# Kernel optimization log

Measured on AMD Instinct MI355X. Metric: run time of the kernel, lower is better.

The kernel has to match this reference:

```python
import jax, jax.numpy as jnp
import numpy as np

K = 5          # k = min(5, min(S, T)) with S = T = 4096
SIGMA = 1.0
EPS_VAR = 1e-08
EPS_LOG = 1e-08


def _entropy(p):
    # sum(-p * log2(clamp(p, 1e-8)), axis=1).mean()
    return jnp.sum(-p * jnp.log2(jnp.clip(p, EPS_LOG, None)), axis=1).mean()


def _pairwise_dist(x):
    # Euclidean cdist via GEMM (matches torch's use_mm_for_euclid path)
    sq = jnp.sum(x * x, axis=1)                       # [N]
    d2 = sq[:, None] + sq[None, :] - 2.0 * (x @ x.T)  # [N, N]
    d2 = jnp.maximum(d2, 0.0)
    # safe sqrt (zero diagonal) — value identical, grad-safe
    return jnp.where(d2 > 0, jnp.sqrt(jnp.where(d2 > 0, d2, 1.0)), 0.0)


def _row_var(block):
    # sqrt(k-th smallest distance per row + eps): max of k smallest
    kth = -jax.lax.top_k(-block, K)[0][:, -1]
    return jnp.sqrt(kth + EPS_VAR)                    # [rows]


def _sim(block, var_row, zero_diag):
    s = jnp.exp(-block / (2.0 * (var_row[:, None] * SIGMA) ** 2))
    if zero_diag:
        n = block.shape[0]
        s = s * (1.0 - jnp.eye(n, dtype=s.dtype))
    return s


def _forward(Feature_all, logit_all, y_source):
    S = y_source.shape[0]
    logit_source = logit_all[:S]
    logit_target = logit_all[S:]

    # cross-entropy on source
    logp = jax.nn.log_softmax(logit_source, axis=1)
    loss_cl = -jnp.take_along_axis(logp, y_source[:, None], axis=1).mean()

    # entropy of target softmax
    loss_ce = _entropy(jax.nn.softmax(logit_target, axis=1))

    # reg_loss_dist
    dist = _pairwise_dist(Feature_all)                # [N, N]
    d_ss = dist[:S, :S]
    d_st = dist[:S, S:]
    d_tt = dist[S:, S:]
    d_ts = dist[S:, :S]

    sim_ss = _sim(d_ss, _row_var(d_ss), True)
    sim_st = _sim(d_st, _row_var(d_st), False)
    sim_tt = _sim(d_tt, _row_var(d_tt), True)
    sim_ts = _sim(d_ts, _row_var(d_ts), False)

    src_intra = jnp.max(sim_ss, axis=1)
    src_inter = jnp.max(sim_st, axis=1)
    tgt_intra = jnp.max(sim_tt, axis=1)
    tgt_inter = jnp.max(sim_ts, axis=1)

    loss_reg = (jnp.abs(src_intra - src_inter).mean()
                + jnp.abs(tgt_intra - tgt_inter).mean())
    return loss_cl, loss_ce, loss_reg


def setup_inputs() -> dict:
    key = jax.random.key(0)
    k1, k2, k3 = jax.random.split(key, 3)
    N, D, C, S = 8192, 256, 65, 4096
    return {
        "Feature_all": jax.random.normal(k1, (N, D), dtype=jnp.float32),
        "logit_all": jax.random.normal(k2, (N, C), dtype=jnp.float32),
        "y_source": jax.random.randint(k3, (S,), 0, C, dtype=jnp.int64
                                       if jax.config.jax_enable_x64 else jnp.int32),
        "device": 0,
    }


def reference(Feature_all, logit_all, y_source, device):
    del device  # torch-specific, ignored
    return _forward(Feature_all, logit_all, y_source)
```

## Files before the change

### kernel.cpp

```cpp
#include <hip/hip_runtime.h>
#include <stdint.h>

#define Nn 8192
#define Dd 256
#define Ss 4096
#define Cc 65

#define TI 128
#define TJ 128
#define BK 32
#define CHUNK 1024
#define NCHUNK (Nn / CHUNK)
#define NJT (CHUNK / TJ)
#define KS (Dd / BK)

#define BIGF 3.0e37f

typedef float f4 __attribute__((ext_vector_type(4)));
typedef __bf16 bf8 __attribute__((ext_vector_type(8)));

__device__ __forceinline__ float wredsum(float v) {
#pragma unroll
  for (int o = 32; o; o >>= 1) v += __shfl_xor(v, o, 64);
  return v;
}
__device__ __forceinline__ float wredmax(float v) {
#pragma unroll
  for (int o = 32; o; o >>= 1) v = fmaxf(v, __shfl_xor(v, o, 64));
  return v;
}

__device__ __forceinline__ unsigned short f2bf(float f) {
  unsigned int u = __float_as_uint(f);
  u = (u + 0x7fffu + ((u >> 16) & 1u)) >> 16;
  return (unsigned short)u;
}

__device__ __forceinline__ void merge5(const float* a, const float* b, float* o) {
  o[0] = fminf(a[0], b[0]);
  o[1] = fminf(fminf(a[1], b[1]), fmaxf(a[0], b[0]));
  o[2] = fminf(fminf(a[2], b[2]), fminf(fmaxf(a[1], b[0]), fmaxf(a[0], b[1])));
  o[3] = fminf(fminf(a[3], b[3]), fminf(fmaxf(a[2], b[0]), fminf(fmaxf(a[1], b[1]), fmaxf(a[0], b[2]))));
  o[4] = fminf(fminf(a[4], b[4]),
               fminf(fmaxf(a[3], b[0]),
                     fminf(fmaxf(a[2], b[1]), fminf(fmaxf(a[1], b[2]), fmaxf(a[0], b[3])))));
}

__global__ __launch_bounds__(256) void prep_loss_kernel(const float* __restrict__ X,
                                                        unsigned short* __restrict__ xb,
                                                        float* __restrict__ sqn,
                                                        const float* __restrict__ logit,
                                                        const int* __restrict__ y,
                                                        float* __restrict__ part_cl,
                                                        float* __restrict__ part_ce,
                                                        unsigned int* __restrict__ counter) {
  if (blockIdx.x == 0 && threadIdx.x == 0) *counter = 0u;
  int lane = threadIdx.x & 63;
  if (blockIdx.x < 2048) {
    int row = blockIdx.x * 4 + (threadIdx.x >> 6);
    f4 v = ((const f4*)(X + (size_t)row * Dd))[lane];
    float ss = v[0] * v[0] + v[1] * v[1] + v[2] * v[2] + v[3] * v[3];
    ss = wredsum(ss);
    if (lane == 0) sqn[row] = ss;
    ushort4 o;
    o.x = f2bf(v[0]); o.y = f2bf(v[1]); o.z = f2bf(v[2]); o.w = f2bf(v[3]);
    ((ushort4*)(xb + (size_t)row * Dd))[lane] = o;
  } else {
    int bid = blockIdx.x - 2048;
    int row = bid * 4 + (threadIdx.x >> 6);
    const float* xr = logit + (size_t)row * Cc;
    float x1 = xr[lane];
    float x2 = (lane == 0) ? xr[64] : -BIGF;
    float mx = wredmax(fmaxf(x1, x2));
    float e1 = expf(x1 - mx);
    float e2 = (lane == 0) ? expf(x2 - mx) : 0.f;
    float Z = wredsum(e1 + e2);
    float res;
    if (row < Ss) {
      int yy = y[row];
      float pick = (lane == yy ? x1 : 0.f) + ((lane == 0 && yy == 64) ? x2 : 0.f);
      float xy = wredsum(pick);
      res = -(xy - mx - logf(Z));
    } else {
      float p1 = e1 / Z;
      float t1 = -p1 * log2f(fmaxf(p1, 1e-8f));
      if (lane == 0) {
        float p2 = e2 / Z;
        t1 += -p2 * log2f(fmaxf(p2, 1e-8f));
      }
      res = wredsum(t1);
    }
    __shared__ float a4[4];
    if (lane == 0) a4[threadIdx.x >> 6] = res;
    __syncthreads();
    if (threadIdx.x == 0) {
      float s = a4[0] + a4[1] + a4[2] + a4[3];
      if (bid < 1024) part_cl[bid] = s;
      else part_ce[bid - 1024] = s;
    }
  }
}

__device__ __forceinline__ void stage16(const void* g, void* l) {
  __builtin_amdgcn_global_load_lds((__attribute__((address_space(1))) void*)g,
                                   (__attribute__((address_space(3))) void*)l, 16, 0, 0);
}

__global__ __launch_bounds__(512, 2) void dist_kernel(const unsigned short* __restrict__ xb,
                                                      const float* __restrict__ sqn,
                                                      float* __restrict__ top5ws) {
  __shared__ unsigned short ldsBuf[2][KS * TI * BK];

  const int tid = threadIdx.x;
  const int lane = tid & 63;
  const int wv = tid >> 6;
  const int q = lane >> 4;
  const int c = lane & 15;
  const int jw = wv & 1;
  const int iq = wv >> 1;

  const int ib = (blockIdx.x / NCHUNK) * TI;
  const int chunk = blockIdx.x % NCHUNK;
  const int jc0 = chunk * CHUNK;

  const int swz = q ^ ((lane >> 1) & 3);
  const int pr = lane >> 2;
  const int qd = (lane & 3) ^ ((lane >> 3) & 3);
  const int gcol = qd * 8;

  float top[2][5];
#pragma unroll
  for (int a = 0; a < 2; ++a)
#pragma unroll
    for (int b = 0; b < 5; ++b) top[a][b] = BIGF;

  const int iwbase = ib + iq * 32;

#pragma unroll
  for (int ks = 0; ks < KS; ++ks) {
    stage16(xb + (size_t)(ib + wv * 16 + pr) * Dd + ks * BK + gcol,
            &ldsBuf[1][ks * (TI * BK) + wv * 512]);
    stage16(xb + (size_t)(jc0 + wv * 16 + pr) * Dd + ks * BK + gcol,
            &ldsBuf[0][ks * (TI * BK) + wv * 512]);
  }
  __syncthreads();

  bf8 bF[KS][2];
#pragma unroll
  for (int ks = 0; ks < KS; ++ks)
#pragma unroll
    for (int ct = 0; ct < 2; ++ct)
      bF[ks][ct] = *(const bf8*)&ldsBuf[1][ks * (TI * BK) + (iq * 32 + ct * 16 + c) * 32 + swz * 8];
  __syncthreads();

  for (int jt = 0; jt < NJT; ++jt) {
    const int jb = jc0 + jt * TJ;
    const int cur = jt & 1;

    if (jt + 1 < NJT) {
      const int jb2 = jb + TJ;
#pragma unroll
      for (int ks = 0; ks < KS; ++ks)
        stage16(xb + (size_t)(jb2 + wv * 16 + pr) * Dd + ks * BK + gcol,
                &ldsBuf[cur ^ 1][ks * (TI * BK) + wv * 512]);
    }

    f4 acc[4][2];
    f4 z = {0.f, 0.f, 0.f, 0.f};
#pragma unroll
    for (int a = 0; a < 4; ++a)
#pragma unroll
      for (int b2 = 0; b2 < 2; ++b2) acc[a][b2] = z;

    const unsigned short* __restrict__ Abase = &ldsBuf[cur][0];
#pragma unroll
    for (int ks = 0; ks < KS; ++ks) {
      bf8 aF[4];
#pragma unroll
      for (int rt = 0; rt < 4; ++rt)
        aF[rt] = *(const bf8*)&Abase[ks * (TI * BK) + (jw * 64 + rt * 16 + c) * 32 + swz * 8];
#pragma unroll
      for (int rt = 0; rt < 4; ++rt)
#pragma unroll
        for (int ct = 0; ct < 2; ++ct)
          acc[rt][ct] = __builtin_amdgcn_mfma_f32_16x16x32_bf16(aF[rt], bF[ks][ct], acc[rt][ct], 0, 0, 0);
    }

    const int jrow = jb + jw * 64;
    f4 sq4[4];
#pragma unroll
    for (int rt = 0; rt < 4; ++rt) sq4[rt] = *(const f4*)&sqn[jrow + rt * 16 + q * 4];
    const bool mayDiag = (jb == ib) && ((iq >> 1) == jw);
#pragma unroll
    for (int ct = 0; ct < 2; ++ct) {
      float t[16];
#pragma unroll
      for (int rt = 0; rt < 4; ++rt)
#pragma unroll
        for (int r = 0; r < 4; ++r)
          t[rt * 4 + r] = fmaf(acc[rt][ct][r], -2.0f, sq4[rt][r]);
      if (mayDiag && ((c >> 2) == q))
        t[((iq & 1) * 2 + ct) * 4 + (c & 3)] = BIGF;
      float tm = fminf(fminf(fminf(fminf(t[0], t[1]), fminf(t[2], t[3])),
                             fminf(fminf(t[4], t[5]), fminf(t[6], t[7]))),
                       fminf(fminf(fminf(t[8], t[9]), fminf(t[10], t[11])),
                             fminf(fminf(t[12], t[13]), fminf(t[14], t[15]))));
      if (tm < top[ct][4]) {
#pragma unroll
        for (int kk = 0; kk < 16; ++kk) {
          float x = t[kk];
          if (x < top[ct][4]) {
#pragma unroll
            for (int s = 0; s < 4; ++s) {
              float lo = fminf(top[ct][s], x);
              x = fmaxf(top[ct][s], x);
              top[ct][s] = lo;
            }
            top[ct][4] = x;
          }
        }
      }
    }
    __syncthreads();
  }

  float fin[2][5];
#pragma unroll
  for (int ct = 0; ct < 2; ++ct) {
    float a0 = top[ct][0], a1 = top[ct][1], a2 = top[ct][2], a3 = top[ct][3], a4 = top[ct][4];
#pragma unroll
    for (int off = 16; off <= 32; off <<= 1) {
      float b0 = __shfl_xor(a0, off, 64);
      float b1 = __shfl_xor(a1, off, 64);
      float b2 = __shfl_xor(a2, off, 64);
      float b3 = __shfl_xor(a3, off, 64);
      float b4 = __shfl_xor(a4, off, 64);
      float c0 = fminf(a0, b0);
      float c1 = fminf(fminf(a1, b1), fmaxf(a0, b0));
      float c2 = fminf(fminf(a2, b2), fminf(fmaxf(a1, b0), fmaxf(a0, b1)));
      float c3 = fminf(fminf(a3, b3), fminf(fmaxf(a2, b0), fminf(fmaxf(a1, b1), fmaxf(a0, b2))));
      float c4 = fminf(fminf(a4, b4),
                       fminf(fmaxf(a3, b0),
                             fminf(fmaxf(a2, b1), fminf(fmaxf(a1, b2), fmaxf(a0, b3)))));
      a0 = c0; a1 = c1; a2 = c2; a3 = c3; a4 = c4;
    }
    fin[ct][0] = a0; fin[ct][1] = a1; fin[ct][2] = a2; fin[ct][3] = a3; fin[ct][4] = a4;
  }

  float* mbuf = (float*)&ldsBuf[0][0];
  if (jw == 1 && q == 0) {
#pragma unroll
    for (int ct = 0; ct < 2; ++ct) {
      float* m = mbuf + ((((iq << 1) | ct) << 4) + c) * 5;
      m[0] = fin[ct][0]; m[1] = fin[ct][1]; m[2] = fin[ct][2]; m[3] = fin[ct][3]; m[4] = fin[ct][4];
    }
  }
  __syncthreads();
  if (jw == 0 && q == 0) {
#pragma unroll
    for (int ct = 0; ct < 2; ++ct) {
      const float* m = mbuf + ((((iq << 1) | ct) << 4) + c) * 5;
      float bl[5] = {m[0], m[1], m[2], m[3], m[4]};
      float o[5];
      merge5(fin[ct], bl, o);
      int i = iwbase + ct * 16 + c;
      float* dst = top5ws + ((size_t)i * NCHUNK + chunk) * 5;
      dst[0] = o[0]; dst[1] = o[1]; dst[2] = o[2]; dst[3] = o[3]; dst[4] = o[4];
    }
  }
}

__device__ __forceinline__ void merge4lists(const float* L, float* o) {
  float m01[5], m23[5];
  merge5(L + 0, L + 5, m01);
  merge5(L + 10, L + 15, m23);
  merge5(m01, m23, o);
}

__global__ __launch_bounds__(256) void reg_final_kernel(const float* __restrict__ top5ws,
                                                        const float* __restrict__ sqn,
                                                        float* __restrict__ part_reg,
                                                        const float* __restrict__ part_cl,
                                                        const float* __restrict__ part_ce,
                                                        float* __restrict__ out,
                                                        unsigned int* __restrict__ counter) {
  int i = blockIdx.x * 256 + threadIdx.x;
  float buf[40];
  const float* L = top5ws + (size_t)i * 40;
#pragma unroll
  for (int k = 0; k < 40; ++k) buf[k] = L[k];
  float mlo[5], mhi[5];
  merge4lists(buf, mlo);
  merge4lists(buf + 20, mhi);
  bool srcRow = (i < Ss);
  float A0 = srcRow ? mlo[0] : mhi[0];
  float A3 = srcRow ? mlo[3] : mhi[3];
  float B0 = srcRow ? mhi[0] : mlo[0];
  float B4 = srcRow ? mhi[4] : mlo[4];
  float sq = sqn[i];
  float dmin_a = sqrtf(fmaxf(A0 + sq, 0.f));
  float kth_a = sqrtf(fmaxf(A3 + sq, 0.f));
  float dmin_b = sqrtf(fmaxf(B0 + sq, 0.f));
  float kth_b = sqrtf(fmaxf(B4 + sq, 0.f));
  float sa = expf(-dmin_a / (2.f * (kth_a + 1e-8f)));
  float sb = expf(-dmin_b / (2.f * (kth_b + 1e-8f)));
  float v = fabsf(sa - sb);
  __shared__ float red[256];
  red[threadIdx.x] = v;
  __syncthreads();
#pragma unroll
  for (int s = 128; s; s >>= 1) {
    if (threadIdx.x < s) red[threadIdx.x] += red[threadIdx.x + s];
    __syncthreads();
  }
  if (threadIdx.x == 0) part_reg[blockIdx.x] = red[0];

  __shared__ unsigned int lastFlag;
  __threadfence();
  if (threadIdx.x == 0) lastFlag = (atomicAdd(counter, 1u) == 31u) ? 1u : 0u;
  __syncthreads();
  if (!lastFlag) return;
  __threadfence();

  __shared__ double dred[256];
  int tid = threadIdx.x;
  double a = 0.0;
  for (int k = tid; k < 1024; k += 256) a += (double)part_cl[k];
  dred[tid] = a; __syncthreads();
  for (int s = 128; s; s >>= 1) { if (tid < s) dred[tid] += dred[tid + s]; __syncthreads(); }
  double cl = dred[0]; __syncthreads();
  a = 0.0;
  for (int k = tid; k < 1024; k += 256) a += (double)part_ce[k];
  dred[tid] = a; __syncthreads();
  for (int s = 128; s; s >>= 1) { if (tid < s) dred[tid] += dred[tid + s]; __syncthreads(); }
  double ce = dred[0]; __syncthreads();
  a = (tid < 16) ? (double)part_reg[tid] : 0.0;
  dred[tid] = a; __syncthreads();
  for (int s = 128; s; s >>= 1) { if (tid < s) dred[tid] += dred[tid + s]; __syncthreads(); }
  double rs = dred[0]; __syncthreads();
  a = (tid >= 16 && tid < 32) ? (double)part_reg[tid] : 0.0;
  dred[tid] = a; __syncthreads();
  for (int s = 128; s; s >>= 1) { if (tid < s) dred[tid] += dred[tid + s]; __syncthreads(); }
  if (tid == 0) {
    out[0] = (float)(cl / 4096.0);
    out[1] = (float)(ce / 4096.0);
    out[2] = (float)(rs / 4096.0 + dred[0] / 4096.0);
  }
}

extern "C" void kernel_launch(void* const* d_in, const int* in_sizes, int n_in,
                              void* d_out, int out_size, void* d_ws, size_t ws_size,
                              hipStream_t stream) {
  (void)in_sizes; (void)n_in; (void)out_size; (void)ws_size;
  const float* X = (const float*)d_in[0];
  const float* logit = (const float*)d_in[1];
  const int* y = (const int*)d_in[2];
  float* out = (float*)d_out;
  char* ws = (char*)d_ws;

  unsigned short* xb = (unsigned short*)ws;
  float* sqn = (float*)(ws + (4u << 20));
  float* top5 = (float*)(ws + (4u << 20) + (64u << 10));
  float* part_cl = (float*)(ws + (7u << 20));
  float* part_ce = part_cl + 1024;
  float* part_reg = part_ce + 1024;
  unsigned int* counter = (unsigned int*)(part_reg + 32);

  hipLaunchKernelGGL(prep_loss_kernel, dim3(4096), dim3(256), 0, stream, X, xb, sqn, logit, y,
                     part_cl, part_ce, counter);
  hipLaunchKernelGGL(dist_kernel, dim3((Nn / TI) * NCHUNK), dim3(512), 0, stream, xb, sqn, top5);
  hipLaunchKernelGGL(reg_final_kernel, dim3(32), dim3(256), 0, stream, top5, sqn, part_reg,
                     part_cl, part_ce, out, counter);
}
```

Measured before the change: 147.5 us.

## Halve dist_kernel LDS footprint with split-K slab double buffering

The LDS tile buffers shrink from full-K double buffers to two half-K slabs, and each j-tile's K loop is split into two halves. The second half of K is staged while the first is computed, and the next tile's first half is staged while the second half is computed. The smaller LDS footprint, together with raising the launch-bounds minimum to 4 blocks, is meant to fit more workgroups per CU and hide latency. In exchange there is an extra barrier per tile, less prefetch distance, and a risk of register spills under the tighter per-thread register budget.

```diff
diff --git a/kernel.cpp b/kernel.cpp
--- a/kernel.cpp
+++ b/kernel.cpp
@@ -13,6 +13,7 @@
 #define NCHUNK (Nn / CHUNK)
 #define NJT (CHUNK / TJ)
 #define KS (Dd / BK)
+#define SLAB (4 * TI * BK)
 
 #define BIGF 3.0e37f
 
@@ -106,10 +107,10 @@
                                    (__attribute__((address_space(3))) void*)l, 16, 0, 0);
 }
 
-__global__ __launch_bounds__(512, 2) void dist_kernel(const unsigned short* __restrict__ xb,
+__global__ __launch_bounds__(512, 4) void dist_kernel(const unsigned short* __restrict__ xb,
                                                       const float* __restrict__ sqn,
                                                       float* __restrict__ top5ws) {
-  __shared__ unsigned short ldsBuf[2][KS * TI * BK];
+  __shared__ unsigned short ldsBuf[2][SLAB];
 
   const int tid = threadIdx.x;
   const int lane = tid & 63;
@@ -137,12 +138,9 @@
   const int iwbase = ib + iq * 32;
 
 #pragma unroll
-  for (int ks = 0; ks < KS; ++ks) {
+  for (int ks = 0; ks < KS; ++ks)
     stage16(xb + (size_t)(ib + wv * 16 + pr) * Dd + ks * BK + gcol,
-            &ldsBuf[1][ks * (TI * BK) + wv * 512]);
-    stage16(xb + (size_t)(jc0 + wv * 16 + pr) * Dd + ks * BK + gcol,
-            &ldsBuf[0][ks * (TI * BK) + wv * 512]);
-  }
+            &ldsBuf[ks >> 2][(ks & 3) * (TI * BK) + wv * 512]);
   __syncthreads();
 
   bf8 bF[KS][2];
@@ -150,20 +148,18 @@
   for (int ks = 0; ks < KS; ++ks)
 #pragma unroll
     for (int ct = 0; ct < 2; ++ct)
-      bF[ks][ct] = *(const bf8*)&ldsBuf[1][ks * (TI * BK) + (iq * 32 + ct * 16 + c) * 32 + swz * 8];
+      bF[ks][ct] = *(const bf8*)&ldsBuf[ks >> 2][(ks & 3) * (TI * BK) +
+                                                 (iq * 32 + ct * 16 + c) * 32 + swz * 8];
+  __syncthreads();
+
+#pragma unroll
+  for (int k2 = 0; k2 < 4; ++k2)
+    stage16(xb + (size_t)(jc0 + wv * 16 + pr) * Dd + k2 * BK + gcol,
+            &ldsBuf[0][k2 * (TI * BK) + wv * 512]);
   __syncthreads();
 
   for (int jt = 0; jt < NJT; ++jt) {
     const int jb = jc0 + jt * TJ;
-    const int cur = jt & 1;
-
-    if (jt + 1 < NJT) {
-      const int jb2 = jb + TJ;
-#pragma unroll
-      for (int ks = 0; ks < KS; ++ks)
-        stage16(xb + (size_t)(jb2 + wv * 16 + pr) * Dd + ks * BK + gcol,
-                &ldsBuf[cur ^ 1][ks * (TI * BK) + wv * 512]);
-    }
 
     f4 acc[4][2];
     f4 z = {0.f, 0.f, 0.f, 0.f};
@@ -172,18 +168,41 @@
 #pragma unroll
       for (int b2 = 0; b2 < 2; ++b2) acc[a][b2] = z;
 
-    const unsigned short* __restrict__ Abase = &ldsBuf[cur][0];
-#pragma unroll
-    for (int ks = 0; ks < KS; ++ks) {
+#pragma unroll
+    for (int k2 = 0; k2 < 4; ++k2)
+      stage16(xb + (size_t)(jb + wv * 16 + pr) * Dd + (4 + k2) * BK + gcol,
+              &ldsBuf[1][k2 * (TI * BK) + wv * 512]);
+#pragma unroll
+    for (int k2 = 0; k2 < 4; ++k2) {
       bf8 aF[4];
 #pragma unroll
       for (int rt = 0; rt < 4; ++rt)
-        aF[rt] = *(const bf8*)&Abase[ks * (TI * BK) + (jw * 64 + rt * 16 + c) * 32 + swz * 8];
+        aF[rt] = *(const bf8*)&ldsBuf[0][k2 * (TI * BK) + (jw * 64 + rt * 16 + c) * 32 + swz * 8];
 #pragma unroll
       for (int rt = 0; rt < 4; ++rt)
 #pragma unroll
         for (int ct = 0; ct < 2; ++ct)
-          acc[rt][ct] = __builtin_amdgcn_mfma_f32_16x16x32_bf16(aF[rt], bF[ks][ct], acc[rt][ct], 0, 0, 0);
+          acc[rt][ct] = __builtin_amdgcn_mfma_f32_16x16x32_bf16(aF[rt], bF[k2][ct], acc[rt][ct], 0, 0, 0);
+    }
+    __syncthreads();
+
+    if (jt + 1 < NJT) {
+#pragma unroll
+      for (int k2 = 0; k2 < 4; ++k2)
+        stage16(xb + (size_t)(jb + TJ + wv * 16 + pr) * Dd + k2 * BK + gcol,
+                &ldsBuf[0][k2 * (TI * BK) + wv * 512]);
+    }
+#pragma unroll
+    for (int k2 = 0; k2 < 4; ++k2) {
+      bf8 aF[4];
+#pragma unroll
+      for (int rt = 0; rt < 4; ++rt)
+        aF[rt] = *(const bf8*)&ldsBuf[1][k2 * (TI * BK) + (jw * 64 + rt * 16 + c) * 32 + swz * 8];
+#pragma unroll
+      for (int rt = 0; rt < 4; ++rt)
+#pragma unroll
+        for (int ct = 0; ct < 2; ++ct)
+          acc[rt][ct] = __builtin_amdgcn_mfma_f32_16x16x32_bf16(aF[rt], bF[4 + k2][ct], acc[rt][ct], 0, 0, 0);
     }
 
     const int jrow = jb + jw * 64;
```

Result: slower. 156.2 us (+5.9%).

## Halve row tile and stream column tiles through K-sliced LDS double buffer

Applied to the files above, without the earlier changes.

Cuts the row tile to 64 with 256-thread blocks and three blocks per CU. Column tiles are no longer double-buffered whole; each is streamed in four K-slices of 64 through a small two-slot LDS buffer, with a barrier after each slice. This shrinks LDS per block to raise occupancy and doubles the grid, at the cost of more frequent barriers and less load lookahead. The diagonal-mask test is rewritten for the new tile shape.

```diff
diff --git a/kernel.cpp b/kernel.cpp
--- a/kernel.cpp
+++ b/kernel.cpp
@@ -6,7 +6,7 @@
 #define Ss 4096
 #define Cc 65
 
-#define TI 128
+#define TI 64
 #define TJ 128
 #define BK 32
 #define CHUNK 1024
@@ -106,10 +106,10 @@
                                    (__attribute__((address_space(3))) void*)l, 16, 0, 0);
 }
 
-__global__ __launch_bounds__(512, 2) void dist_kernel(const unsigned short* __restrict__ xb,
+__global__ __launch_bounds__(256, 3) void dist_kernel(const unsigned short* __restrict__ xb,
                                                       const float* __restrict__ sqn,
                                                       float* __restrict__ top5ws) {
-  __shared__ unsigned short ldsBuf[2][KS * TI * BK];
+  __shared__ unsigned short ldsBuf[2][2 * TJ * BK];
 
   const int tid = threadIdx.x;
   const int lane = tid & 63;
@@ -127,6 +127,7 @@
   const int pr = lane >> 2;
   const int qd = (lane & 3) ^ ((lane >> 3) & 3);
   const int gcol = qd * 8;
+  const int u0 = wv * 2, u1 = wv * 2 + 1;
 
   float top[2][5];
 #pragma unroll
@@ -136,13 +137,11 @@
 
   const int iwbase = ib + iq * 32;
 
-#pragma unroll
-  for (int ks = 0; ks < KS; ++ks) {
+  unsigned short* ldsB = &ldsBuf[0][0];
+#pragma unroll
+  for (int ks = 0; ks < KS; ++ks)
     stage16(xb + (size_t)(ib + wv * 16 + pr) * Dd + ks * BK + gcol,
-            &ldsBuf[1][ks * (TI * BK) + wv * 512]);
-    stage16(xb + (size_t)(jc0 + wv * 16 + pr) * Dd + ks * BK + gcol,
-            &ldsBuf[0][ks * (TI * BK) + wv * 512]);
-  }
+            &ldsB[ks * (TI * BK) + wv * 512]);
   __syncthreads();
 
   bf8 bF[KS][2];
@@ -150,20 +149,20 @@
   for (int ks = 0; ks < KS; ++ks)
 #pragma unroll
     for (int ct = 0; ct < 2; ++ct)
-      bF[ks][ct] = *(const bf8*)&ldsBuf[1][ks * (TI * BK) + (iq * 32 + ct * 16 + c) * 32 + swz * 8];
+      bF[ks][ct] = *(const bf8*)&ldsB[ks * (TI * BK) + (iq * 32 + ct * 16 + c) * 32 + swz * 8];
+  __syncthreads();
+
+#pragma unroll
+  for (int sl = 0; sl < 2; ++sl) {
+    stage16(xb + (size_t)(jc0 + u0 * 16 + pr) * Dd + sl * BK + gcol,
+            &ldsBuf[0][sl * (TJ * BK) + u0 * 512]);
+    stage16(xb + (size_t)(jc0 + u1 * 16 + pr) * Dd + sl * BK + gcol,
+            &ldsBuf[0][sl * (TJ * BK) + u1 * 512]);
+  }
   __syncthreads();
 
   for (int jt = 0; jt < NJT; ++jt) {
     const int jb = jc0 + jt * TJ;
-    const int cur = jt & 1;
-
-    if (jt + 1 < NJT) {
-      const int jb2 = jb + TJ;
-#pragma unroll
-      for (int ks = 0; ks < KS; ++ks)
-        stage16(xb + (size_t)(jb2 + wv * 16 + pr) * Dd + ks * BK + gcol,
-                &ldsBuf[cur ^ 1][ks * (TI * BK) + wv * 512]);
-    }
 
     f4 acc[4][2];
     f4 z = {0.f, 0.f, 0.f, 0.f};
@@ -172,25 +171,42 @@
 #pragma unroll
       for (int b2 = 0; b2 < 2; ++b2) acc[a][b2] = z;
 
-    const unsigned short* __restrict__ Abase = &ldsBuf[cur][0];
-#pragma unroll
-    for (int ks = 0; ks < KS; ++ks) {
-      bf8 aF[4];
-#pragma unroll
-      for (int rt = 0; rt < 4; ++rt)
-        aF[rt] = *(const bf8*)&Abase[ks * (TI * BK) + (jw * 64 + rt * 16 + c) * 32 + swz * 8];
-#pragma unroll
-      for (int rt = 0; rt < 4; ++rt)
-#pragma unroll
-        for (int ct = 0; ct < 2; ++ct)
-          acc[rt][ct] = __builtin_amdgcn_mfma_f32_16x16x32_bf16(aF[rt], bF[ks][ct], acc[rt][ct], 0, 0, 0);
+#pragma unroll
+    for (int pp = 0; pp < 4; ++pp) {
+      if (!((jt == NJT - 1) && (pp == 3))) {
+        const int nb = (pp == 3) ? jb + TJ : jb;
+        const int nk = ((pp == 3) ? 0 : (pp + 1) * 2) * BK;
+#pragma unroll
+        for (int sl = 0; sl < 2; ++sl) {
+          stage16(xb + (size_t)(nb + u0 * 16 + pr) * Dd + nk + sl * BK + gcol,
+                  &ldsBuf[(pp & 1) ^ 1][sl * (TJ * BK) + u0 * 512]);
+          stage16(xb + (size_t)(nb + u1 * 16 + pr) * Dd + nk + sl * BK + gcol,
+                  &ldsBuf[(pp & 1) ^ 1][sl * (TJ * BK) + u1 * 512]);
+        }
+      }
+#pragma unroll
+      for (int sl = 0; sl < 2; ++sl) {
+        bf8 aF[4];
+#pragma unroll
+        for (int rt = 0; rt < 4; ++rt)
+          aF[rt] = *(const bf8*)&ldsBuf[pp & 1][sl * (TJ * BK) +
+                                               (jw * 64 + rt * 16 + c) * 32 + swz * 8];
+#pragma unroll
+        for (int rt = 0; rt < 4; ++rt)
+#pragma unroll
+          for (int ct = 0; ct < 2; ++ct)
+            acc[rt][ct] = __builtin_amdgcn_mfma_f32_16x16x32_bf16(aF[rt], bF[pp * 2 + sl][ct],
+                                                                  acc[rt][ct], 0, 0, 0);
+      }
+      __syncthreads();
     }
 
     const int jrow = jb + jw * 64;
     f4 sq4[4];
 #pragma unroll
     for (int rt = 0; rt < 4; ++rt) sq4[rt] = *(const f4*)&sqn[jrow + rt * 16 + q * 4];
-    const bool mayDiag = (jb == ib) && ((iq >> 1) == jw);
+    const int dif = iwbase - jrow;
+    const bool mayDiag = (dif == 0) || (dif == 32);
 #pragma unroll
     for (int ct = 0; ct < 2; ++ct) {
       float t[16];
@@ -200,7 +216,7 @@
         for (int r = 0; r < 4; ++r)
           t[rt * 4 + r] = fmaf(acc[rt][ct][r], -2.0f, sq4[rt][r]);
       if (mayDiag && ((c >> 2) == q))
-        t[((iq & 1) * 2 + ct) * 4 + (c & 3)] = BIGF;
+        t[((dif >> 4) + ct) * 4 + (c & 3)] = BIGF;
       float tm = fminf(fminf(fminf(fminf(t[0], t[1]), fminf(t[2], t[3])),
                              fminf(fminf(t[4], t[5]), fminf(t[6], t[7]))),
                        fminf(fminf(fminf(t[8], t[9]), fminf(t[10], t[11])),
@@ -221,7 +237,6 @@
         }
       }
     }
-    __syncthreads();
   }
 
   float fin[2][5];
@@ -368,7 +383,7 @@
 
   hipLaunchKernelGGL(prep_loss_kernel, dim3(4096), dim3(256), 0, stream, X, xb, sqn, logit, y,
                      part_cl, part_ce, counter);
-  hipLaunchKernelGGL(dist_kernel, dim3((Nn / TI) * NCHUNK), dim3(512), 0, stream, xb, sqn, top5);
+  hipLaunchKernelGGL(dist_kernel, dim3((Nn / TI) * NCHUNK), dim3(256), 0, stream, xb, sqn, top5);
   hipLaunchKernelGGL(reg_final_kernel, dim3(32), dim3(256), 0, stream, top5, sqn, part_reg,
                      part_cl, part_ce, out, counter);
 }
```

Result: faster. 143.3 us (-2.9%).
